# Kernel tuning notes

Measured on AMD Instinct MI355X. Metric: run time of the kernel, lower is better.

## Reference

```python
import jax, jax.numpy as jnp
import numpy as np
import math

D_MODEL = 1024
NUM_HEADS = 16
D_K = D_MODEL // NUM_HEADS
THETA = 10000.0
BATCH = 2
SEQ = 2048


def _trunc_normal(key, shape, std):
    # truncated normal in [-3std, 3std], matching torch.nn.init.trunc_normal_
    return jax.random.truncated_normal(key, -3.0, 3.0, shape, jnp.float32) * std


def setup_inputs() -> dict:
    key = jax.random.key(0)
    kx, kq, kk, kv, ko = jax.random.split(key, 5)
    std = math.sqrt(2.0 / (D_MODEL + D_MODEL))
    return {
        "x": jax.random.normal(kx, (BATCH, SEQ, D_MODEL), jnp.float32),
        "Wq": _trunc_normal(kq, (D_MODEL, D_MODEL), std),
        "Wk": _trunc_normal(kk, (D_MODEL, D_MODEL), std),
        "Wv": _trunc_normal(kv, (D_MODEL, D_MODEL), std),
        "Wo": _trunc_normal(ko, (D_MODEL, D_MODEL), std),
    }


def _apply_rope(t):
    # t: [B, H, S, d_k]; positions = arange(S)
    S = t.shape[-2]
    inv_freq = 1.0 / THETA ** (jnp.arange(0, D_K, 2, dtype=jnp.float32) / D_K)
    ang = jnp.arange(S, dtype=jnp.float32)[:, None] * inv_freq[None, :]  # [S, d_k/2]
    cos, sin = jnp.cos(ang), jnp.sin(ang)
    t1 = t[..., ::2]
    t2 = t[..., 1::2]
    r1 = t1 * cos - t2 * sin
    r2 = t1 * sin + t2 * cos
    # interleave back: even indices <- r1, odd <- r2
    out = jnp.stack([r1, r2], axis=-1).reshape(t.shape)
    return out


def reference(x, Wq, Wk, Wv, Wo):
    B, S, _ = x.shape
    def proj(W):
        return (x @ W.T).reshape(B, S, NUM_HEADS, D_K).transpose(0, 2, 1, 3)
    q = _apply_rope(proj(Wq))
    k = _apply_rope(proj(Wk))
    v = proj(Wv)
    scores = jnp.einsum('bhqd,bhkd->bhqk', q, k) / math.sqrt(D_K)
    causal = jnp.tril(jnp.ones((S, S), dtype=bool))
    scores = jnp.where(causal, scores, -jnp.inf)
    attn = jax.nn.softmax(scores, axis=-1)
    ctx = jnp.einsum('bhqk,bhkd->bhqd', attn, v)  # [B,H,S,d_k]
    ctx = ctx.transpose(0, 2, 1, 3).reshape(B, S, D_MODEL)
    return ctx @ Wo.T
```

## Files before the change

### kernel.cpp

```cpp
#include <hip/hip_runtime.h>
#include <hip/hip_bf16.h>


typedef __attribute__((ext_vector_type(8))) short bf16x8;
typedef __attribute__((ext_vector_type(4))) short bf16x4;
typedef __attribute__((ext_vector_type(4))) float f32x4;

#define D_MODEL 1024
#define SEQ     2048
#define NHEAD   16
#define DK      64
#define EXP_BIAS 16.0f

__device__ __forceinline__ f32x4 mfma16(bf16x8 a, bf16x8 b, f32x4 c) {
    return __builtin_amdgcn_mfma_f32_16x16x32_bf16(a, b, c, 0, 0, 0);
}

__device__ __forceinline__ void load_lds16(const __hip_bfloat16* g, __hip_bfloat16* l) {
    __builtin_amdgcn_global_load_lds((const __attribute__((address_space(1))) void*)g,
                                     (__attribute__((address_space(3))) void*)l,
                                     16, 0, 0);
}

__device__ __forceinline__ void cvt8(const float* p, __hip_bfloat16* dst) {
    const float4 f0 = *(const float4*)p;
    const float4 f1 = *(const float4*)(p + 4);
    alignas(16) __hip_bfloat16 t[8] = {
        __float2bfloat16(f0.x), __float2bfloat16(f0.y),
        __float2bfloat16(f0.z), __float2bfloat16(f0.w),
        __float2bfloat16(f1.x), __float2bfloat16(f1.y),
        __float2bfloat16(f1.z), __float2bfloat16(f1.w)};
    *(bf16x8*)dst = *(const bf16x8*)t;
}

__global__ __launch_bounds__(256) void cvt5_k(const float* __restrict__ wq,
                                              const float* __restrict__ wk,
                                              const float* __restrict__ wv,
                                              const float* __restrict__ wo,
                                              const float* __restrict__ x,
                                              __hip_bfloat16* __restrict__ dw,
                                              __hip_bfloat16* __restrict__ dwo,
                                              __hip_bfloat16* __restrict__ dx) {
    const int id = blockIdx.x;
    const float* s;
    __hip_bfloat16* d;
    int off;
    if (id < 1536)      { const int w = id >> 9; s = (w == 0) ? wq : (w == 1 ? wk : wv);
                          d = dw + (size_t)w * 1024 * 1024; off = (id & 511) * 2048; }
    else if (id < 2048) { s = wo; d = dwo; off = (id - 1536) * 2048; }
    else                { s = x;  d = dx;  off = (id - 2048) * 2048; }
    const int i = off + threadIdx.x * 8;
    alignas(16) __hip_bfloat16 t[8];
    cvt8(s + i, t);
    *(bf16x8*)(d + i) = *(const bf16x8*)t;
}

__global__ __launch_bounds__(256) void cvt3_k(const float* __restrict__ s0,
                                              const float* __restrict__ s1,
                                              const float* __restrict__ s2,
                                              __hip_bfloat16* __restrict__ d0,
                                              __hip_bfloat16* __restrict__ d1,
                                              __hip_bfloat16* __restrict__ d2) {
    const float* s = (blockIdx.y == 0) ? s0 : (blockIdx.y == 1 ? s1 : s2);
    __hip_bfloat16* d = (blockIdx.y == 0) ? d0 : (blockIdx.y == 1 ? d1 : d2);
    const int i = (blockIdx.x * 256 + threadIdx.x) * 8;
    alignas(16) __hip_bfloat16 t[8];
    cvt8(s + i, t);
    *(bf16x8*)(d + i) = *(const bf16x8*)t;
}

__device__ __forceinline__ void qkv_epilogue(f32x4 (&acc)[4][4], int wsel,
                                             int bm, int bn, int wave,
                                             int quad, int l15,
                                             __hip_bfloat16* Cq,
                                             __hip_bfloat16* Ck,
                                             __hip_bfloat16* Vt) {
    if (wsel < 2) {
        __hip_bfloat16* C = (wsel == 0) ? Cq : Ck;
#pragma unroll
        for (int i = 0; i < 4; ++i)
#pragma unroll
            for (int j = 0; j < 4; ++j)
#pragma unroll
                for (int r = 0; r < 4; ++r) {
                    const int row = bm + (wave >> 1) * 64 + i * 16 + quad * 4 + r;
                    const int col = bn + (wave & 1) * 64 + j * 16 + l15;
                    C[(size_t)row * 1024 + col] = __float2bfloat16(acc[i][j][r]);
                }
    } else {
#pragma unroll
        for (int i = 0; i < 4; ++i)
#pragma unroll
            for (int j = 0; j < 4; ++j) {
                const int col  = bn + (wave & 1) * 64 + j * 16 + l15;
                const int hh   = col >> 6, dd = col & 63;
                const int row0 = bm + (wave >> 1) * 64 + i * 16 + quad * 4;
                const int bb   = row0 >> 11, s0 = row0 & 2047;
                alignas(8) __hip_bfloat16 t4[4] = {
                    __float2bfloat16(acc[i][j][0]), __float2bfloat16(acc[i][j][1]),
                    __float2bfloat16(acc[i][j][2]), __float2bfloat16(acc[i][j][3])};
                *(uint2*)&Vt[((size_t)(bb * 16 + hh) * 64 + dd) * 2048 + s0] =
                    *(const uint2*)t4;
            }
    }
}

__global__ __launch_bounds__(256) void gemm_qkv_bf(const __hip_bfloat16* __restrict__ X,
                                                   const __hip_bfloat16* __restrict__ W,
                                                   __hip_bfloat16* __restrict__ Cq,
                                                   __hip_bfloat16* __restrict__ Ck,
                                                   __hip_bfloat16* __restrict__ Vt) {
    __shared__ alignas(16) __hip_bfloat16 a_lds[2][128 * 32];
    __shared__ alignas(16) __hip_bfloat16 b_lds[2][128 * 32];

    const int tid  = threadIdx.x;
    const int wave = tid >> 6;
    const int lane = tid & 63;
    const int quad = lane >> 4;
    const int l15  = lane & 15;

    const int wsel = blockIdx.x >> 3;
    const int bn   = (blockIdx.x & 7) * 128;
    const int bm   = blockIdx.y * 128;

    const __hip_bfloat16* Bw = W + (size_t)wsel * 1024 * 1024;

    f32x4 acc[4][4] = {};

    const int chunk0 = (wave * 2 + 0) * 64 + lane;
    const int chunk1 = (wave * 2 + 1) * 64 + lane;
    const int row0 = chunk0 >> 2, c0 = chunk0 & 3;
    const int row1 = chunk1 >> 2, c1 = chunk1 & 3;
    const int col0 = (c0 ^ (row0 & 3)) * 8;
    const int col1 = (c1 ^ (row1 & 3)) * 8;

    auto stage = [&](int buf, int k0) {
        load_lds16(&X [(size_t)(bm + row0) * 1024 + k0 + col0], &a_lds[buf][(wave * 2 + 0) * 512]);
        load_lds16(&Bw[(size_t)(bn + row0) * 1024 + k0 + col0], &b_lds[buf][(wave * 2 + 0) * 512]);
        load_lds16(&X [(size_t)(bm + row1) * 1024 + k0 + col1], &a_lds[buf][(wave * 2 + 1) * 512]);
        load_lds16(&Bw[(size_t)(bn + row1) * 1024 + k0 + col1], &b_lds[buf][(wave * 2 + 1) * 512]);
    };

    const int sw8 = (quad ^ (l15 & 3)) * 8;

    auto compute = [&](int buf) {
        bf16x8 af[4], bfr[4];
#pragma unroll
        for (int i = 0; i < 4; ++i)
            af[i] = *(const bf16x8*)&a_lds[buf][((wave >> 1) * 64 + i * 16 + l15) * 32 + sw8];
#pragma unroll
        for (int j = 0; j < 4; ++j)
            bfr[j] = *(const bf16x8*)&b_lds[buf][((wave & 1) * 64 + j * 16 + l15) * 32 + sw8];
#pragma unroll
        for (int i = 0; i < 4; ++i)
#pragma unroll
            for (int j = 0; j < 4; ++j)
                acc[i][j] = mfma16(af[i], bfr[j], acc[i][j]);
    };

    stage(0, 0);
    stage(1, 32);

#pragma unroll 1
    for (int tt = 0; tt < 16; ++tt) {
        const int k0 = tt * 64;

        asm volatile("s_waitcnt vmcnt(4)" ::: "memory");
        __builtin_amdgcn_s_barrier();
        __builtin_amdgcn_sched_barrier(0);
        compute(0);
        __builtin_amdgcn_sched_barrier(0);
        __builtin_amdgcn_s_barrier();
        if (tt < 15) stage(0, k0 + 64);

        if (tt < 15) { asm volatile("s_waitcnt vmcnt(4)" ::: "memory"); }
        else         { asm volatile("s_waitcnt vmcnt(0)" ::: "memory"); }
        __builtin_amdgcn_s_barrier();
        __builtin_amdgcn_sched_barrier(0);
        compute(1);
        __builtin_amdgcn_sched_barrier(0);
        __builtin_amdgcn_s_barrier();
        if (tt < 15) stage(1, k0 + 96);
    }

    qkv_epilogue(acc, wsel, bm, bn, wave, quad, l15, Cq, Ck, Vt);
}

__global__ __launch_bounds__(256) void gemm_qkv_f32(const float* __restrict__ X,
                                                    const __hip_bfloat16* __restrict__ W,
                                                    __hip_bfloat16* __restrict__ Cq,
                                                    __hip_bfloat16* __restrict__ Ck,
                                                    __hip_bfloat16* __restrict__ Vt) {
    __shared__ alignas(16) __hip_bfloat16 a_lds[128 * 32];
    __shared__ alignas(16) __hip_bfloat16 b_lds[128 * 32];

    const int tid  = threadIdx.x;
    const int wave = tid >> 6;
    const int lane = tid & 63;
    const int quad = lane >> 4;
    const int l15  = lane & 15;

    const int wsel = blockIdx.x >> 3;
    const int bn   = (blockIdx.x & 7) * 128;
    const int bm   = blockIdx.y * 128;

    const __hip_bfloat16* B = W + (size_t)wsel * 1024 * 1024;

    f32x4 acc[4][4] = {};

    for (int k0 = 0; k0 < 1024; k0 += 32) {
        __syncthreads();
#pragma unroll
        for (int c = 0; c < 2; ++c) {
            const int e   = (c * 256 + tid) * 8;
            const int row = e >> 5;
            const int col = e & 31;
            cvt8(&X[(size_t)(bm + row) * 1024 + k0 + col], &a_lds[e]);
        }
#pragma unroll
        for (int c = 0; c < 2; ++c) {
            const int chunk = (wave * 2 + c) * 64 + lane;
            const int row = chunk >> 2;
            const int col = (chunk & 3) * 8;
            load_lds16(&B[(size_t)(bn + row) * 1024 + k0 + col],
                       &b_lds[(wave * 2 + c) * 512]);
        }
        __syncthreads();

        bf16x8 af[4], bfr[4];
#pragma unroll
        for (int i = 0; i < 4; ++i)
            af[i] = *(const bf16x8*)&a_lds[((wave >> 1) * 64 + i * 16 + l15) * 32 + quad * 8];
#pragma unroll
        for (int j = 0; j < 4; ++j)
            bfr[j] = *(const bf16x8*)&b_lds[((wave & 1) * 64 + j * 16 + l15) * 32 + quad * 8];
#pragma unroll
        for (int i = 0; i < 4; ++i)
#pragma unroll
            for (int j = 0; j < 4; ++j)
                acc[i][j] = mfma16(af[i], bfr[j], acc[i][j]);
    }

    qkv_epilogue(acc, wsel, bm, bn, wave, quad, l15, Cq, Ck, Vt);
}

__global__ __launch_bounds__(256) void gemm_o(const __hip_bfloat16* __restrict__ A,
                                              const __hip_bfloat16* __restrict__ B,
                                              float* __restrict__ C) {
    __shared__ alignas(16) __hip_bfloat16 a_lds[2][128 * 32];
    __shared__ alignas(16) __hip_bfloat16 b_lds[2][64 * 32];

    const int tid  = threadIdx.x;
    const int wave = tid >> 6;
    const int lane = tid & 63;
    const int quad = lane >> 4;
    const int l15  = lane & 15;

    const int bn = blockIdx.x * 64;
    const int bm = blockIdx.y * 128;

    f32x4 acc[2][4] = {};

    auto stage = [&](int buf, int k0) {
#pragma unroll
        for (int c = 0; c < 2; ++c) {
            const int chunk = (wave * 2 + c) * 64 + lane;
            const int row = chunk >> 2;
            const int col = (chunk & 3) * 8;
            load_lds16(&A[(size_t)(bm + row) * 1024 + k0 + col],
                       &a_lds[buf][(wave * 2 + c) * 512]);
        }
        {
            const int chunk = wave * 64 + lane;
            const int row = chunk >> 2;
            const int col = (chunk & 3) * 8;
            load_lds16(&B[(size_t)(bn + row) * 1024 + k0 + col],
                       &b_lds[buf][wave * 512]);
        }
    };

    stage(0, 0);
    __syncthreads();

    for (int k0 = 0; k0 < 1024; k0 += 32) {
        const int buf = (k0 >> 5) & 1;
        if (k0 + 32 < 1024) stage(buf ^ 1, k0 + 32);

        bf16x8 af[2], bfr[4];
#pragma unroll
        for (int i = 0; i < 2; ++i)
            af[i] = *(const bf16x8*)&a_lds[buf][(wave * 32 + i * 16 + l15) * 32 + quad * 8];
#pragma unroll
        for (int j = 0; j < 4; ++j)
            bfr[j] = *(const bf16x8*)&b_lds[buf][(j * 16 + l15) * 32 + quad * 8];
#pragma unroll
        for (int i = 0; i < 2; ++i)
#pragma unroll
            for (int j = 0; j < 4; ++j)
                acc[i][j] = mfma16(af[i], bfr[j], acc[i][j]);

        __syncthreads();
    }

#pragma unroll
    for (int i = 0; i < 2; ++i)
#pragma unroll
        for (int j = 0; j < 4; ++j)
#pragma unroll
            for (int r = 0; r < 4; ++r) {
                const int row = bm + wave * 32 + i * 16 + quad * 4 + r;
                const int col = bn + j * 16 + l15;
                C[(size_t)row * 1024 + col] = acc[i][j][r];
            }
}

__global__ __launch_bounds__(256) void rope_k(__hip_bfloat16* Q, __hip_bfloat16* K) {
    const int idx = blockIdx.x * 256 + threadIdx.x;
    const int row = idx >> 7;
    const int g   = idx & 127;
    const int col = g * 8;
    const int s   = row & (SEQ - 1);
    const int i0  = (g & 7) * 4;

    float sn[4], cs[4];
#pragma unroll
    for (int z = 0; z < 4; ++z) {
        const float ang = (float)s * __expf(-(float)(i0 + z) * 0.28782313663f);
        __sincosf(ang, &sn[z], &cs[z]);
    }

    const size_t o = (size_t)row * D_MODEL + col;
    alignas(16) __hip_bfloat16 q8[8], k8[8];
    *(uint4*)q8 = *(const uint4*)&Q[o];
    *(uint4*)k8 = *(const uint4*)&K[o];
#pragma unroll
    for (int z = 0; z < 4; ++z) {
        const float q1 = __bfloat162float(q8[2 * z]);
        const float q2 = __bfloat162float(q8[2 * z + 1]);
        q8[2 * z]     = __float2bfloat16((q1 * cs[z] - q2 * sn[z]) * 0.125f);
        q8[2 * z + 1] = __float2bfloat16((q1 * sn[z] + q2 * cs[z]) * 0.125f);
        const float k1 = __bfloat162float(k8[2 * z]);
        const float k2 = __bfloat162float(k8[2 * z + 1]);
        k8[2 * z]     = __float2bfloat16(k1 * cs[z] - k2 * sn[z]);
        k8[2 * z + 1] = __float2bfloat16(k1 * sn[z] + k2 * cs[z]);
    }
    *(uint4*)&Q[o] = *(const uint4*)q8;
    *(uint4*)&K[o] = *(const uint4*)k8;
}

__global__ __launch_bounds__(256, 4) void attn_k(const __hip_bfloat16* Q,
                                                 const __hip_bfloat16* K,
                                                 const __hip_bfloat16* Vt,
                                                 __hip_bfloat16* O) {
    __shared__ alignas(16) __hip_bfloat16 k_s[2][64 * 72];
    __shared__ alignas(16) __hip_bfloat16 vt_s[2][64 * 72];

    const int tid  = threadIdx.x;
    const int wave = tid >> 6;
    const int lane = tid & 63;
    const int quad = lane >> 4;
    const int l15  = lane & 15;

    const int hw = blockIdx.x;
    const int j  = hw >> 3;
    const int g  = j >> 5;
    const int m  = j & 31;
    const int bh = (hw & 7) * 4 + g;
    const int mm = (g >= 2) ? ((m + 8) & 31) : m;
    const int qt = (g & 1) ? mm : (31 - mm);
    const int b  = bh >> 4;
    const int h  = bh & 15;
    const int q0 = qt * 64;

    const int r0 = tid >> 3;
    const int d8 = (tid & 7) * 8;
    const int vp0 = ((d8 >> 5) << 5) + (((d8 & 15) >> 2) << 3) + (((d8 >> 4) & 1) << 2);
    const int d4  = d8 + 4;
    const int vp1 = ((d4 >> 5) << 5) + (((d4 & 15) >> 2) << 3) + (((d4 >> 4) & 1) << 2);

    const size_t vtBase = (size_t)bh * (64 * 2048);
    const size_t baseK0 = ((size_t)(b * SEQ)) * D_MODEL + h * DK;

#pragma unroll
    for (int c = 0; c < 2; ++c) {
        const int row = r0 + c * 32;
        const uint4 kv = *(const uint4*)&K[baseK0 + (size_t)row * D_MODEL + d8];
        const uint4 vv = *(const uint4*)&Vt[vtBase + (size_t)row * 2048 + d8];
        *(uint4*)&k_s[0][row * 72 + d8] = kv;
        uint2 lo, hi;
        lo.x = vv.x; lo.y = vv.y; hi.x = vv.z; hi.y = vv.w;
        *(uint2*)&vt_s[0][row * 72 + vp0] = lo;
        *(uint2*)&vt_s[0][row * 72 + vp1] = hi;
    }

    bf16x8 qa0, qa1;
    {
        const size_t baseQ = ((size_t)(b * SEQ + q0 + wave * 16 + l15)) * D_MODEL + h * DK;
        qa0 = *(const bf16x8*)&Q[baseQ + quad * 8];
        qa1 = *(const bf16x8*)&Q[baseQ + 32 + quad * 8];
    }
    __syncthreads();

    float l4[4] = {0.f, 0.f, 0.f, 0.f};
    f32x4 o_acc[4] = {};

    for (int kt = 0; kt < qt; ++kt) {
        const int buf = kt & 1;

        uint4 kr0, kr1, vr0, vr1;
        {
            const size_t baseK = baseK0 + (size_t)(kt + 1) * 64 * D_MODEL;
            const size_t baseV = vtBase + (size_t)(kt + 1) * 64;
            kr0 = *(const uint4*)&K[baseK + (size_t)r0 * D_MODEL + d8];
            kr1 = *(const uint4*)&K[baseK + (size_t)(r0 + 32) * D_MODEL + d8];
            vr0 = *(const uint4*)&Vt[baseV + (size_t)r0 * 2048 + d8];
            vr1 = *(const uint4*)&Vt[baseV + (size_t)(r0 + 32) * 2048 + d8];
        }

        alignas(16) __hip_bfloat16 pk0[8], pk1[8];
#pragma unroll
        for (int t = 0; t < 4; ++t) {
            __hip_bfloat16* dst = (t < 2) ? pk0 : pk1;
            const int zo = (t & 1) * 4;
            f32x4 a = {};
            __builtin_amdgcn_s_setprio(1);
            const bf16x8 kb0 = *(const bf16x8*)&k_s[buf][(t * 16 + l15) * 72 + quad * 8];
            a = mfma16(kb0, qa0, a);
            const bf16x8 kb1 = *(const bf16x8*)&k_s[buf][(t * 16 + l15) * 72 + 32 + quad * 8];
            a = mfma16(kb1, qa1, a);
            __builtin_amdgcn_s_setprio(0);
#pragma unroll
            for (int r = 0; r < 4; ++r) {
                const float pv = __expf(a[r] - EXP_BIAS);
                l4[r] += pv;
                dst[zo + r] = __float2bfloat16(pv);
            }
        }
        const bf16x8 pa0 = *(const bf16x8*)pk0;
        const bf16x8 pa1 = *(const bf16x8*)pk1;

        __builtin_amdgcn_s_setprio(1);
#pragma unroll
        for (int ks = 0; ks < 2; ++ks) {
            const bf16x8 pa = ks ? pa1 : pa0;
#pragma unroll
            for (int t2 = 0; t2 < 4; ++t2) {
                const bf16x8 vv = *(const bf16x8*)
                    &vt_s[buf][(t2 * 16 + l15) * 72 + ks * 32 + quad * 8];
                o_acc[t2] = mfma16(pa, vv, o_acc[t2]);
            }
        }
        __builtin_amdgcn_s_setprio(0);

        *(uint4*)&k_s[buf ^ 1][r0 * 72 + d8] = kr0;
        *(uint4*)&k_s[buf ^ 1][(r0 + 32) * 72 + d8] = kr1;
        {
            uint2 lo0, hi0, lo1, hi1;
            lo0.x = vr0.x; lo0.y = vr0.y; hi0.x = vr0.z; hi0.y = vr0.w;
            lo1.x = vr1.x; lo1.y = vr1.y; hi1.x = vr1.z; hi1.y = vr1.w;
            *(uint2*)&vt_s[buf ^ 1][r0 * 72 + vp0] = lo0;
            *(uint2*)&vt_s[buf ^ 1][r0 * 72 + vp1] = hi0;
            *(uint2*)&vt_s[buf ^ 1][(r0 + 32) * 72 + vp0] = lo1;
            *(uint2*)&vt_s[buf ^ 1][(r0 + 32) * 72 + vp1] = hi1;
        }

        __syncthreads();
    }

    {
        const int buf = qt & 1;
        alignas(16) __hip_bfloat16 pk0[8], pk1[8];
#pragma unroll
        for (int t = 0; t < 4; ++t) {
            __hip_bfloat16* dst = (t < 2) ? pk0 : pk1;
            const int zo = (t & 1) * 4;
            if (t > wave) {
#pragma unroll
                for (int r = 0; r < 4; ++r) dst[zo + r] = __float2bfloat16(0.0f);
                continue;
            }
            f32x4 a = {};
            const bf16x8 kb0 = *(const bf16x8*)&k_s[buf][(t * 16 + l15) * 72 + quad * 8];
            a = mfma16(kb0, qa0, a);
            const bf16x8 kb1 = *(const bf16x8*)&k_s[buf][(t * 16 + l15) * 72 + 32 + quad * 8];
            a = mfma16(kb1, qa1, a);
#pragma unroll
            for (int r = 0; r < 4; ++r) {
                float v = a[r];
                if (t == wave && (quad * 4 + r > l15)) v = -1e30f;
                const float pv = __expf(v - EXP_BIAS);
                l4[r] += pv;
                dst[zo + r] = __float2bfloat16(pv);
            }
        }
        const bf16x8 pa0 = *(const bf16x8*)pk0;
        const bf16x8 pa1 = *(const bf16x8*)pk1;

#pragma unroll
        for (int ks = 0; ks < 2; ++ks) {
            if (ks == 1 && wave < 2) continue;
            const bf16x8 pa = ks ? pa1 : pa0;
#pragma unroll
            for (int t2 = 0; t2 < 4; ++t2) {
                const bf16x8 vv = *(const bf16x8*)
                    &vt_s[buf][(t2 * 16 + l15) * 72 + ks * 32 + quad * 8];
                o_acc[t2] = mfma16(pa, vv, o_acc[t2]);
            }
        }
    }

    float l_loc = (l4[0] + l4[1]) + (l4[2] + l4[3]);
    l_loc += __shfl_xor(l_loc, 16);
    l_loc += __shfl_xor(l_loc, 32);
    float lr[4];
#pragma unroll
    for (int r = 0; r < 4; ++r) lr[r] = __shfl(l_loc, quad * 4 + r);

#pragma unroll
    for (int t2 = 0; t2 < 4; ++t2)
#pragma unroll
        for (int r = 0; r < 4; ++r) {
            const int row = q0 + wave * 16 + quad * 4 + r;
            const int d   = t2 * 16 + l15;
            O[((size_t)(b * SEQ + row)) * D_MODEL + h * DK + d] =
                __float2bfloat16(o_acc[t2][r] / lr[r]);
        }
}

extern "C" void kernel_launch(void* const* d_in, const int* in_sizes, int n_in,
                              void* d_out, int out_size, void* d_ws, size_t ws_size,
                              hipStream_t stream) {
    const float* x  = (const float*)d_in[0];
    const float* Wq = (const float*)d_in[1];
    const float* Wk = (const float*)d_in[2];
    const float* Wv = (const float*)d_in[3];
    const float* Wo = (const float*)d_in[4];

    const size_t MT = (size_t)4096 * 1024;
    const size_t WT = (size_t)1024 * 1024;
    __hip_bfloat16* Qw = (__hip_bfloat16*)d_ws;
    __hip_bfloat16* Vt = Qw + MT;
    __hip_bfloat16* Wb = (__hip_bfloat16*)d_out;
    __hip_bfloat16* Kw = (__hip_bfloat16*)((char*)d_out + 8 * 1024 * 1024);

    const bool big = ws_size >= (size_t)26 * 1024 * 1024;

    if (big) {
        __hip_bfloat16* xb  = Qw + 2 * MT;
        __hip_bfloat16* WoB = (__hip_bfloat16*)((char*)d_ws + 24 * 1024 * 1024);
        cvt5_k<<<4096, 256, 0, stream>>>(Wq, Wk, Wv, Wo, x, Wb, WoB, xb);
        gemm_qkv_bf<<<dim3(24, 32), 256, 0, stream>>>(xb, Wb, Qw, Kw, Vt);
        rope_k<<<(4096 * 128) / 256, 256, 0, stream>>>(Qw, Kw);
        attn_k<<<dim3(1024), 256, 0, stream>>>(Qw, Kw, Vt, Qw);
        gemm_o<<<dim3(16, 32), 256, 0, stream>>>(Qw, WoB, (float*)d_out);
    } else {
        __hip_bfloat16* WoB = Vt;
        cvt3_k<<<dim3(512, 3), 256, 0, stream>>>(Wq, Wk, Wv, Wb, Wb + WT, Wb + 2 * WT);
        gemm_qkv_f32<<<dim3(24, 32), 256, 0, stream>>>(x, Wb, Qw, Kw, Vt);
        rope_k<<<(4096 * 128) / 256, 256, 0, stream>>>(Qw, Kw);
        attn_k<<<dim3(1024), 256, 0, stream>>>(Qw, Kw, Vt, Qw);
        cvt3_k<<<dim3(512, 1), 256, 0, stream>>>(Wo, Wo, Wo, WoB, WoB, WoB);
        gemm_o<<<dim3(16, 32), 256, 0, stream>>>(Qw, WoB, (float*)d_out);
    }
}
```

Before: 184.6 us.

## Fuse Q RoPE into attention load and swizzle/pipeline output GEMM LDS

RoPE for Q is now applied inside the attention kernel when Q fragments are loaded, so the standalone rope kernel only rotates K and the Q read/write pass over memory is gone. Separately, the output-projection GEMM gets an XOR-swizzled LDS layout to cut bank conflicts, plus a two-stage manually unrolled pipeline with explicit vmcnt waits and raw barriers. The attention kernel now does extra sincos/exp work per block for Q, and the hand-written waitcnt counts tie correctness to the exact number of outstanding loads.

```diff
diff --git a/kernel.cpp b/kernel.cpp
--- a/kernel.cpp
+++ b/kernel.cpp
@@ -11,6 +11,7 @@
 #define NHEAD   16
 #define DK      64
 #define EXP_BIAS 16.0f
+#define ROPE_LN  0.28782313663f
 
 __device__ __forceinline__ f32x4 mfma16(bf16x8 a, bf16x8 b, f32x4 c) {
     return __builtin_amdgcn_mfma_f32_16x16x32_bf16(a, b, c, 0, 0, 0);
@@ -261,45 +262,62 @@
 
     f32x4 acc[2][4] = {};
 
+    const int chunkA0 = (wave * 2 + 0) * 64 + lane;
+    const int chunkA1 = (wave * 2 + 1) * 64 + lane;
+    const int rA0 = chunkA0 >> 2, cA0 = chunkA0 & 3;
+    const int rA1 = chunkA1 >> 2, cA1 = chunkA1 & 3;
+    const int colA0 = (cA0 ^ (rA0 & 3)) * 8;
+    const int colA1 = (cA1 ^ (rA1 & 3)) * 8;
+    const int chunkB = wave * 64 + lane;
+    const int rB = chunkB >> 2, cB = chunkB & 3;
+    const int colB = (cB ^ (rB & 3)) * 8;
+
     auto stage = [&](int buf, int k0) {
-#pragma unroll
-        for (int c = 0; c < 2; ++c) {
-            const int chunk = (wave * 2 + c) * 64 + lane;
-            const int row = chunk >> 2;
-            const int col = (chunk & 3) * 8;
-            load_lds16(&A[(size_t)(bm + row) * 1024 + k0 + col],
-                       &a_lds[buf][(wave * 2 + c) * 512]);
-        }
-        {
-            const int chunk = wave * 64 + lane;
-            const int row = chunk >> 2;
-            const int col = (chunk & 3) * 8;
-            load_lds16(&B[(size_t)(bn + row) * 1024 + k0 + col],
-                       &b_lds[buf][wave * 512]);
-        }
+        load_lds16(&A[(size_t)(bm + rA0) * 1024 + k0 + colA0], &a_lds[buf][(wave * 2 + 0) * 512]);
+        load_lds16(&A[(size_t)(bm + rA1) * 1024 + k0 + colA1], &a_lds[buf][(wave * 2 + 1) * 512]);
+        load_lds16(&B[(size_t)(bn + rB) * 1024 + k0 + colB],   &b_lds[buf][wave * 512]);
     };
 
-    stage(0, 0);
-    __syncthreads();
-
-    for (int k0 = 0; k0 < 1024; k0 += 32) {
-        const int buf = (k0 >> 5) & 1;
-        if (k0 + 32 < 1024) stage(buf ^ 1, k0 + 32);
-
+    const int sw8 = (quad ^ (l15 & 3)) * 8;
+
+    auto compute = [&](int buf) {
         bf16x8 af[2], bfr[4];
 #pragma unroll
         for (int i = 0; i < 2; ++i)
-            af[i] = *(const bf16x8*)&a_lds[buf][(wave * 32 + i * 16 + l15) * 32 + quad * 8];
+            af[i] = *(const bf16x8*)&a_lds[buf][(wave * 32 + i * 16 + l15) * 32 + sw8];
 #pragma unroll
         for (int j = 0; j < 4; ++j)
-            bfr[j] = *(const bf16x8*)&b_lds[buf][(j * 16 + l15) * 32 + quad * 8];
+            bfr[j] = *(const bf16x8*)&b_lds[buf][(j * 16 + l15) * 32 + sw8];
 #pragma unroll
         for (int i = 0; i < 2; ++i)
 #pragma unroll
             for (int j = 0; j < 4; ++j)
                 acc[i][j] = mfma16(af[i], bfr[j], acc[i][j]);
-
-        __syncthreads();
+    };
+
+    stage(0, 0);
+    stage(1, 32);
+
+#pragma unroll 1
+    for (int tt = 0; tt < 16; ++tt) {
+        const int k0 = tt * 64;
+
+        asm volatile("s_waitcnt vmcnt(3)" ::: "memory");
+        __builtin_amdgcn_s_barrier();
+        __builtin_amdgcn_sched_barrier(0);
+        compute(0);
+        __builtin_amdgcn_sched_barrier(0);
+        __builtin_amdgcn_s_barrier();
+        if (tt < 15) stage(0, k0 + 64);
+
+        if (tt < 15) { asm volatile("s_waitcnt vmcnt(3)" ::: "memory"); }
+        else         { asm volatile("s_waitcnt vmcnt(0)" ::: "memory"); }
+        __builtin_amdgcn_s_barrier();
+        __builtin_amdgcn_sched_barrier(0);
+        compute(1);
+        __builtin_amdgcn_sched_barrier(0);
+        __builtin_amdgcn_s_barrier();
+        if (tt < 15) stage(1, k0 + 96);
     }
 
 #pragma unroll
@@ -314,7 +332,7 @@
             }
 }
 
-__global__ __launch_bounds__(256) void rope_k(__hip_bfloat16* Q, __hip_bfloat16* K) {
+__global__ __launch_bounds__(256) void ropek_k(__hip_bfloat16* K) {
     const int idx = blockIdx.x * 256 + threadIdx.x;
     const int row = idx >> 7;
     const int g   = idx & 127;
@@ -325,26 +343,20 @@
     float sn[4], cs[4];
 #pragma unroll
     for (int z = 0; z < 4; ++z) {
-        const float ang = (float)s * __expf(-(float)(i0 + z) * 0.28782313663f);
+        const float ang = (float)s * __expf(-(float)(i0 + z) * ROPE_LN);
         __sincosf(ang, &sn[z], &cs[z]);
     }
 
     const size_t o = (size_t)row * D_MODEL + col;
-    alignas(16) __hip_bfloat16 q8[8], k8[8];
-    *(uint4*)q8 = *(const uint4*)&Q[o];
+    alignas(16) __hip_bfloat16 k8[8];
     *(uint4*)k8 = *(const uint4*)&K[o];
 #pragma unroll
     for (int z = 0; z < 4; ++z) {
-        const float q1 = __bfloat162float(q8[2 * z]);
-        const float q2 = __bfloat162float(q8[2 * z + 1]);
-        q8[2 * z]     = __float2bfloat16((q1 * cs[z] - q2 * sn[z]) * 0.125f);
-        q8[2 * z + 1] = __float2bfloat16((q1 * sn[z] + q2 * cs[z]) * 0.125f);
         const float k1 = __bfloat162float(k8[2 * z]);
         const float k2 = __bfloat162float(k8[2 * z + 1]);
         k8[2 * z]     = __float2bfloat16(k1 * cs[z] - k2 * sn[z]);
         k8[2 * z + 1] = __float2bfloat16(k1 * sn[z] + k2 * cs[z]);
     }
-    *(uint4*)&Q[o] = *(const uint4*)q8;
     *(uint4*)&K[o] = *(const uint4*)k8;
 }
 
@@ -395,9 +407,30 @@
 
     bf16x8 qa0, qa1;
     {
-        const size_t baseQ = ((size_t)(b * SEQ + q0 + wave * 16 + l15)) * D_MODEL + h * DK;
-        qa0 = *(const bf16x8*)&Q[baseQ + quad * 8];
-        qa1 = *(const bf16x8*)&Q[baseQ + 32 + quad * 8];
+        const int srow = q0 + wave * 16 + l15;
+        const size_t baseQ = ((size_t)(b * SEQ + srow)) * D_MODEL + h * DK;
+        bf16x8 raw0 = *(const bf16x8*)&Q[baseQ + quad * 8];
+        bf16x8 raw1 = *(const bf16x8*)&Q[baseQ + 32 + quad * 8];
+        alignas(16) __hip_bfloat16 t0[8], t1[8], o0[8], o1[8];
+        *(bf16x8*)t0 = raw0;
+        *(bf16x8*)t1 = raw1;
+#pragma unroll
+        for (int u = 0; u < 4; ++u) {
+            const int ip0 = quad * 4 + u;
+            float sn0, cs0, sn1, cs1;
+            __sincosf((float)srow * __expf(-(float)ip0 * ROPE_LN), &sn0, &cs0);
+            __sincosf((float)srow * __expf(-(float)(16 + ip0) * ROPE_LN), &sn1, &cs1);
+            const float a1 = __bfloat162float(t0[2 * u]);
+            const float a2 = __bfloat162float(t0[2 * u + 1]);
+            o0[2 * u]     = __float2bfloat16((a1 * cs0 - a2 * sn0) * 0.125f);
+            o0[2 * u + 1] = __float2bfloat16((a1 * sn0 + a2 * cs0) * 0.125f);
+            const float b1 = __bfloat162float(t1[2 * u]);
+            const float b2 = __bfloat162float(t1[2 * u + 1]);
+            o1[2 * u]     = __float2bfloat16((b1 * cs1 - b2 * sn1) * 0.125f);
+            o1[2 * u + 1] = __float2bfloat16((b1 * sn1 + b2 * cs1) * 0.125f);
+        }
+        qa0 = *(const bf16x8*)o0;
+        qa1 = *(const bf16x8*)o1;
     }
     __syncthreads();
 
@@ -550,14 +583,14 @@
         __hip_bfloat16* WoB = (__hip_bfloat16*)((char*)d_ws + 24 * 1024 * 1024);
         cvt5_k<<<4096, 256, 0, stream>>>(Wq, Wk, Wv, Wo, x, Wb, WoB, xb);
         gemm_qkv_bf<<<dim3(24, 32), 256, 0, stream>>>(xb, Wb, Qw, Kw, Vt);
-        rope_k<<<(4096 * 128) / 256, 256, 0, stream>>>(Qw, Kw);
+        ropek_k<<<(4096 * 128) / 256, 256, 0, stream>>>(Kw);
         attn_k<<<dim3(1024), 256, 0, stream>>>(Qw, Kw, Vt, Qw);
         gemm_o<<<dim3(16, 32), 256, 0, stream>>>(Qw, WoB, (float*)d_out);
     } else {
         __hip_bfloat16* WoB = Vt;
         cvt3_k<<<dim3(512, 3), 256, 0, stream>>>(Wq, Wk, Wv, Wb, Wb + WT, Wb + 2 * WT);
         gemm_qkv_f32<<<dim3(24, 32), 256, 0, stream>>>(x, Wb, Qw, Kw, Vt);
-        rope_k<<<(4096 * 128) / 256, 256, 0, stream>>>(Qw, Kw);
+        ropek_k<<<(4096 * 128) / 256, 256, 0, stream>>>(Kw);
         attn_k<<<dim3(1024), 256, 0, stream>>>(Qw, Kw, Vt, Qw);
         cvt3_k<<<dim3(512, 1), 256, 0, stream>>>(Wo, Wo, Wo, WoB, WoB, WoB);
         gemm_o<<<dim3(16, 32), 256, 0, stream>>>(Qw, WoB, (float*)d_out);
```

Result: faster. 177.3 us (-4.0%).
